# Kernel optimization log

Measured on AMD Instinct MI355X. Metric: run time of the kernel, lower is better.

Reference implementation:

```python
import jax, jax.numpy as jnp
import numpy as np

N = 20000      # nodes
E = 320000     # edges (before self loops)
IN = 128       # in_channels
HID = 64       # hid_channels
H = 4          # in_head
OUT = 16       # out_channels (classes)
SLOPE = 0.2    # GATv2 leaky_relu negative_slope default


def setup_inputs() -> dict:
    key = jax.random.key(0)
    ks = jax.random.split(key, 40)
    d = {}
    d["x"] = jax.random.normal(ks[0], (N, IN), jnp.float32)
    src = jax.random.randint(ks[1], (E,), 0, N)
    dst = jax.random.randint(ks[2], (E,), 0, N)
    d["edge_index"] = jnp.stack([src, dst]).astype(jnp.int32)
    # (in_ch, out_ch_per_head, heads) for the 4 GATv2Conv layers
    dims = [(IN, HID, H), (H * HID, HID, H), (H * HID, HID, H), (H * HID, OUT, 1)]
    ki = 3
    for li, (ic, oc, h) in enumerate(dims, 1):
        sc = 1.0 / np.sqrt(ic)
        d[f"w{li}l"] = jax.random.normal(ks[ki], (h * oc, ic), jnp.float32) * sc; ki += 1
        d[f"b{li}l"] = jnp.zeros((h * oc,), jnp.float32)
        d[f"w{li}r"] = jax.random.normal(ks[ki], (h * oc, ic), jnp.float32) * sc; ki += 1
        d[f"b{li}r"] = jnp.zeros((h * oc,), jnp.float32)
        d[f"a{li}"] = jax.random.normal(ks[ki], (h, oc), jnp.float32) * (1.0 / np.sqrt(oc)); ki += 1
        # output bias: [h*oc] if concat else [oc]; layer 4 is concat=False
        d[f"bo{li}"] = jnp.zeros((h * oc if li < 4 else oc,), jnp.float32)
    return d


def gatv2_layer(x, src, dst, wl, bl, wr, br, att, bias, heads, oc, concat):
    n = x.shape[0]
    xl = (x @ wl.T + bl).reshape(n, heads, oc)   # source transform
    xr = (x @ wr.T + br).reshape(n, heads, oc)   # target transform
    # per-edge GATv2 attention logit: a^T LeakyReLU(x_l[src] + x_r[dst])
    e = jax.nn.leaky_relu(xl[src] + xr[dst], SLOPE)          # [E,H,C]
    logits = jnp.einsum('ehc,hc->eh', e, att)                # [E,H]
    # segment softmax over incoming edges of each dst node
    m = jax.ops.segment_max(logits, dst, num_segments=n)     # [N,H]
    ex = jnp.exp(logits - m[dst])
    den = jax.ops.segment_sum(ex, dst, num_segments=n)
    alpha = ex / den[dst]                                    # [E,H]
    out = jax.ops.segment_sum(alpha[..., None] * xl[src], dst, num_segments=n)  # [N,H,C]
    out = out.reshape(n, heads * oc) if concat else out.mean(axis=1)
    return out + bias


def reference(x, edge_index,
              w1l, b1l, w1r, b1r, a1, bo1,
              w2l, b2l, w2r, b2r, a2, bo2,
              w3l, b3l, w3r, b3r, a3, bo3,
              w4l, b4l, w4r, b4r, a4, bo4):
    n = x.shape[0]
    loop = jnp.arange(n, dtype=edge_index.dtype)
    src = jnp.concatenate([edge_index[0], loop])  # PyG GATv2Conv adds self loops
    dst = jnp.concatenate([edge_index[1], loop])
    h = gatv2_layer(x, src, dst, w1l, b1l, w1r, b1r, a1, bo1, H, HID, True)
    h = jax.nn.relu(h)
    h = gatv2_layer(h, src, dst, w2l, b2l, w2r, b2r, a2, bo2, H, HID, True)
    h = jax.nn.relu(h)
    h = gatv2_layer(h, src, dst, w3l, b3l, w3r, b3r, a3, bo3, H, HID, True)
    h = jax.nn.relu(h)
    h = gatv2_layer(h, src, dst, w4l, b4l, w4r, b4r, a4, bo4, 1, OUT, False)
    return h
```

## Files before the change

kernel.cpp:

```cpp
#include <hip/hip_runtime.h>
#include <hip/hip_bf16.h>
#include <math.h>

#define NNODES 20000
#define NEDGES 320000
#define ETOT   (NEDGES + NNODES)
#define SLOPE  0.2f
#define MAXDEG 96

typedef __attribute__((ext_vector_type(8))) short bf16x8;
typedef __attribute__((ext_vector_type(4))) float f32x4;

__device__ inline unsigned short bfbits(float f) {
    __hip_bfloat16 h = __float2bfloat16(f);
    unsigned short u;
    __builtin_memcpy(&u, &h, 2);
    return u;
}
__device__ inline float bf2f(unsigned short u) {
    __hip_bfloat16 h;
    __builtin_memcpy(&h, &u, 2);
    return __bfloat162float(h);
}

__device__ inline void gload_lds16(const unsigned short* g, unsigned short* s) {
    __builtin_amdgcn_global_load_lds(
        (const __attribute__((address_space(1))) unsigned int*)g,
        (__attribute__((address_space(3))) unsigned int*)s, 16, 0, 0);
}

__global__ void slab_fill(const int* __restrict__ ei, int* __restrict__ fill,
                          int* __restrict__ slab) {
    int idx = blockIdx.x * blockDim.x + threadIdx.x;
    if (idx >= ETOT) return;
    int src, dst;
    if (idx < NEDGES) { src = ei[idx]; dst = ei[NEDGES + idx]; }
    else              { src = idx - NEDGES; dst = src; }
    int pos = atomicAdd(&fill[dst], 1);
    if (pos < MAXDEG) slab[dst * MAXDEG + pos] = src;
}

__global__ void bin_hist(const int* __restrict__ fill, int* __restrict__ bcnt) {
    __shared__ int h[32];
    const int t = threadIdx.x;
    if (t < 32) h[t] = 0;
    __syncthreads();
    int n = blockIdx.x * 256 + t;
    if (n < NNODES) atomicAdd(&h[min(fill[n], 31)], 1);
    __syncthreads();
    if (t < 32 && h[t] > 0) atomicAdd(&bcnt[t], h[t]);
}

__global__ void bin_scan(const int* __restrict__ bcnt, int* __restrict__ bfill) {
    if (threadIdx.x == 0) {
        int run = 0;
        for (int i = 0; i < 32; i++) { bfill[i] = run; run += bcnt[i]; }
    }
}

__global__ void bin_place(const int* __restrict__ fill, int* __restrict__ bfill,
                          int* __restrict__ order) {
    __shared__ int h[32];
    __shared__ int base[32];
    const int t = threadIdx.x;
    if (t < 32) h[t] = 0;
    __syncthreads();
    int n = blockIdx.x * 256 + t;
    int bin = 0, loc = 0;
    if (n < NNODES) {
        bin = min(fill[n], 31);
        loc = atomicAdd(&h[bin], 1);
    }
    __syncthreads();
    if (t < 32) base[t] = (h[t] > 0) ? atomicAdd(&bfill[t], h[t]) : 0;
    __syncthreads();
    if (n < NNODES) order[base[bin] + loc] = n;
}

__global__ void convert_x(const float* __restrict__ x, unsigned short* __restrict__ Ap) {
    int idx = blockIdx.x * 256 + threadIdx.x;
    if (idx >= NNODES * 128) return;
    int m = idx >> 7, k = idx & 127;
    float f = x[idx];
    unsigned short hi = bfbits(f);
    unsigned short lo = bfbits(f - bf2f(hi));
    unsigned short* row = Ap + (size_t)m * 256;
    row[k] = hi; row[128 + k] = lo;
}

__global__ void convert_w(const float* __restrict__ w0, const float* __restrict__ w1,
                          unsigned short* __restrict__ Wp, int K, int n0, int ntot) {
    int idx = blockIdx.x * 256 + threadIdx.x;
    if (idx >= ntot * K) return;
    int n = idx / K, k = idx - n * K;
    float f = (n < n0) ? w0[n * K + k] : w1[(n - n0) * K + k];
    unsigned short hi = bfbits(f);
    unsigned short lo = bfbits(f - bf2f(hi));
    unsigned short* row = Wp + (size_t)n * 2 * K;
    row[k] = hi; row[K + k] = lo;
}

template <int NOUT>
__global__ __launch_bounds__(256) void gemm_mfma(
    const unsigned short* __restrict__ Ap, int KK,
    const unsigned short* __restrict__ Wp,
    const float* __restrict__ bias0, const float* __restrict__ bias1,
    float* __restrict__ O0, float* __restrict__ O1)
{
    __shared__ unsigned short AH[2 * 4096];
    __shared__ unsigned short AL[2 * 4096];
    __shared__ unsigned short BH[2 * 4096];
    __shared__ unsigned short BL[2 * 4096];

    int m0, nblk;
    if constexpr (NOUT == 512) {
        const int bid = blockIdx.x;
        const int xcd = bid & 7;
        const int k   = bid >> 3;
        nblk = k & 3;
        const int g = (k >> 2) * 8 + xcd;
        if (g >= (NNODES + 127) / 128) return;
        m0 = g * 128;
    } else {
        nblk = 0;
        m0 = blockIdx.x * 128;
    }
    const int n0 = nblk * 128;

    const int tid = threadIdx.x;
    const int l   = tid & 63;
    const int wid = tid >> 6;
    const int wr  = wid >> 1;
    const int wc  = wid & 1;

    const int srow = l & 15;
    const int skb  = l >> 4;
    const int W2K  = 2 * KK;

    int arow0 = m0 + wid * 16 + srow;
    int arow1 = arow0 + 64;
    arow0 = min(arow0, NNODES - 1);
    arow1 = min(arow1, NNODES - 1);
    const unsigned short* ahg0 = Ap + (size_t)arow0 * W2K + skb * 8;
    const unsigned short* ahg1 = Ap + (size_t)arow1 * W2K + skb * 8;
    int nrow0 = min(n0 + wid * 16 + srow, NOUT - 1);
    int nrow1 = min(n0 + wid * 16 + srow + 64, NOUT - 1);
    const unsigned short* bhg0 = Wp + (size_t)nrow0 * W2K + skb * 8;
    const unsigned short* bhg1 = Wp + (size_t)nrow1 * W2K + skb * 8;

    const int f0 = (0 * 4 + wid) * 512;
    const int f1 = (1 * 4 + wid) * 512;

    f32x4 acc[4][4];
    #pragma unroll
    for (int i = 0; i < 4; i++)
        #pragma unroll
        for (int j = 0; j < 4; j++)
            acc[i][j] = (f32x4){0.f, 0.f, 0.f, 0.f};

    const int S = KK >> 5;

    auto STAGE = [&](int buf, int k0) {
        const int bo = buf * 4096;
        gload_lds16(ahg0 + k0,      &AH[bo + f0]);
        gload_lds16(ahg1 + k0,      &AH[bo + f1]);
        gload_lds16(ahg0 + KK + k0, &AL[bo + f0]);
        gload_lds16(ahg1 + KK + k0, &AL[bo + f1]);
        gload_lds16(bhg0 + k0,      &BH[bo + f0]);
        gload_lds16(bhg1 + k0,      &BH[bo + f1]);
        gload_lds16(bhg0 + KK + k0, &BL[bo + f0]);
        gload_lds16(bhg1 + KK + k0, &BL[bo + f1]);
    };

    const int ra = (wr * 4) * 512 + l * 8;
    const int rb = (wc * 4) * 512 + l * 8;

    STAGE(0, 0);
    __syncthreads();

    int cur = 0;
    for (int s = 0; s < S; ++s) {
        if (s + 1 < S) STAGE(cur ^ 1, (s + 1) * 32);

        const int bo = cur * 4096;
        bf16x8 ah[4], al_[4], bh[4], bl[4];
        #pragma unroll
        for (int i = 0; i < 4; i++) {
            ah[i]  = *(const bf16x8*)&AH[bo + ra + i * 512];
            al_[i] = *(const bf16x8*)&AL[bo + ra + i * 512];
            bh[i]  = *(const bf16x8*)&BH[bo + rb + i * 512];
            bl[i]  = *(const bf16x8*)&BL[bo + rb + i * 512];
        }

        #pragma unroll
        for (int mi = 0; mi < 4; mi++)
            #pragma unroll
            for (int ni = 0; ni < 4; ni++) {
                acc[mi][ni] = __builtin_amdgcn_mfma_f32_16x16x32_bf16(ah[mi],  bh[ni], acc[mi][ni], 0, 0, 0);
                acc[mi][ni] = __builtin_amdgcn_mfma_f32_16x16x32_bf16(ah[mi],  bl[ni], acc[mi][ni], 0, 0, 0);
                acc[mi][ni] = __builtin_amdgcn_mfma_f32_16x16x32_bf16(al_[mi], bh[ni], acc[mi][ni], 0, 0, 0);
            }

        __syncthreads();
        cur ^= 1;
    }

    if constexpr (NOUT == 512) {
        const bool  left = (nblk < 2);
        float*       O   = left ? O0 : O1;
        const float* bs  = left ? bias0 : bias1;
        const int   cb   = (nblk & 1) * 128;
        #pragma unroll
        for (int mi = 0; mi < 4; mi++) {
            int r0 = m0 + wr * 64 + mi * 16 + (l >> 4) * 4;
            #pragma unroll
            for (int ni = 0; ni < 4; ni++) {
                int c = cb + wc * 64 + ni * 16 + (l & 15);
                int head = c >> 6, ch = c & 63;
                float bv = bs[c];
                #pragma unroll
                for (int r = 0; r < 4; r++) {
                    int m = r0 + r;
                    if (m < NNODES)
                        O[((size_t)head * NNODES + m) * 64 + ch] = acc[mi][ni][r] + bv;
                }
            }
        }
    } else {
        #pragma unroll
        for (int mi = 0; mi < 4; mi++) {
            int r0 = m0 + wr * 64 + mi * 16 + (l >> 4) * 4;
            #pragma unroll
            for (int ni = 0; ni < 4; ni++) {
                int c = wc * 64 + ni * 16 + (l & 15);
                if (c >= 32) continue;
                float bv = (c < 16) ? bias0[c] : bias1[c - 16];
                #pragma unroll
                for (int r = 0; r < 4; r++) {
                    int m = r0 + r;
                    if (m < NNODES) O0[(size_t)m * 32 + c] = acc[mi][ni][r] + bv;
                }
            }
        }
    }
}

__device__ inline float edge_score(float4 v, float4 xrv, float4 attv) {
    float tx = v.x + xrv.x; tx = fmaxf(tx, SLOPE * tx);
    float ty = v.y + xrv.y; ty = fmaxf(ty, SLOPE * ty);
    float tz = v.z + xrv.z; tz = fmaxf(tz, SLOPE * tz);
    float tw = v.w + xrv.w; tw = fmaxf(tw, SLOPE * tw);
    float s = attv.x * tx + attv.y * ty + attv.z * tz + attv.w * tw;
    s += __shfl_xor(s, 1, 64);
    s += __shfl_xor(s, 2, 64);
    s += __shfl_xor(s, 4, 64);
    s += __shfl_xor(s, 8, 64);
    return s;
}

__device__ inline void sm_upd(float s, float4 v, bool act,
                              float& m, float& den, float4& acc) {
    float d = s - m;
    bool  r = act && (d > 8.f);
    float e = __expf(r ? -d : d);
    float sc = r ? e : 1.f;
    float pw = act ? (r ? 1.f : e) : 0.f;
    m = r ? s : m;
    den = den * sc + pw;
    acc.x = acc.x * sc + pw * v.x;
    acc.y = acc.y * sc + pw * v.y;
    acc.z = acc.z * sc + pw * v.z;
    acc.w = acc.w * sc + pw * v.w;
}

__device__ inline void sm_merge(float& m0, float& den0, float4& acc0,
                                float m1, float den1, float4 acc1) {
    float nm = fmaxf(m0, m1);
    float sa = __expf(m0 - nm);
    float sb = __expf(m1 - nm);
    den0 = den0 * sa + den1 * sb;
    acc0.x = acc0.x * sa + acc1.x * sb;
    acc0.y = acc0.y * sa + acc1.y * sb;
    acc0.z = acc0.z * sa + acc1.z * sb;
    acc0.w = acc0.w * sa + acc1.w * sb;
    m0 = nm;
}

__global__ __launch_bounds__(64) void gat_attn_head(
    const float* __restrict__ xl, const float* __restrict__ xr,
    const float* __restrict__ att, const float* __restrict__ bo,
    const int* __restrict__ fill, const int* __restrict__ slab,
    const int* __restrict__ order,
    unsigned short* __restrict__ outp)
{
    const int b    = blockIdx.x;
    const int xcd  = b & 7;
    const int head = xcd >> 1;
    const int grp  = (b >> 3) * 2 + (xcd & 1);
    const int lane = threadIdx.x;
    const int sub  = lane >> 4;
    const int c    = lane & 15;

    const int node = order[grp * 4 + sub];
    const unsigned coff = (unsigned)c << 4;

    const char* xlh = (const char*)xl + (size_t)head * (NNODES * 256);
    const char* xrh = (const char*)xr + (size_t)head * (NNODES * 256);

    const float4 attv = *(const float4*)&att[head * 64 + c * 4];
    const float4 xrv  = *(const float4*)(xrh + ((unsigned)node << 8) + coff);
    const float4 bov  = *(const float4*)&bo[head * 64 + c * 4];

    const int  deg = min(fill[node], MAXDEG);
    const int* sl  = slab + node * MAXDEG;

    int maxd = deg;
    maxd = max(maxd, __shfl_xor(maxd, 16, 64));
    maxd = max(maxd, __shfl_xor(maxd, 32, 64));

    float  m0 = -1e30f, m1 = -1e30f, m2 = -1e30f, m3 = -1e30f;
    float  d0 = 0.f, d1 = 0.f, d2 = 0.f, d3 = 0.f;
    float4 a0 = make_float4(0.f, 0.f, 0.f, 0.f);
    float4 a1 = a0, a2 = a0, a3 = a0;

    auto gather = [&](int src) -> float4 {
        return *(const float4*)(xlh + (((unsigned)src << 8) + coff));
    };

    auto batch = [&](float4 v0, float4 v1, float4 v2, float4 v3, int pb) {
        const bool A0 = pb + 0 < deg, A1 = pb + 1 < deg;
        const bool A2 = pb + 2 < deg, A3 = pb + 3 < deg;
        float s0 = edge_score(v0, xrv, attv);
        float s1 = edge_score(v1, xrv, attv);
        float s2 = edge_score(v2, xrv, attv);
        float s3 = edge_score(v3, xrv, attv);
        bool need = (A0 & (s0 - m0 > 8.f)) | (A1 & (s1 - m1 > 8.f)) |
                    (A2 & (s2 - m2 > 8.f)) | (A3 & (s3 - m3 > 8.f));
        if (!__any(need)) {
            float p0 = A0 ? __expf(s0 - m0) : 0.f;
            float p1 = A1 ? __expf(s1 - m1) : 0.f;
            float p2 = A2 ? __expf(s2 - m2) : 0.f;
            float p3 = A3 ? __expf(s3 - m3) : 0.f;
            d0 += p0; d1 += p1; d2 += p2; d3 += p3;
            a0.x += p0 * v0.x; a0.y += p0 * v0.y; a0.z += p0 * v0.z; a0.w += p0 * v0.w;
            a1.x += p1 * v1.x; a1.y += p1 * v1.y; a1.z += p1 * v1.z; a1.w += p1 * v1.w;
            a2.x += p2 * v2.x; a2.y += p2 * v2.y; a2.z += p2 * v2.z; a2.w += p2 * v2.w;
            a3.x += p3 * v3.x; a3.y += p3 * v3.y; a3.z += p3 * v3.z; a3.w += p3 * v3.w;
        } else {
            sm_upd(s0, v0, A0, m0, d0, a0);
            sm_upd(s1, v1, A1, m1, d1, a1);
            sm_upd(s2, v2, A2, m2, d2, a2);
            sm_upd(s3, v3, A3, m3, d3, a3);
        }
    };

    int4 s4 = *(const int4*)sl;
    float4 v0 = gather((0 < deg) ? s4.x : node);
    float4 v1 = gather((1 < deg) ? s4.y : node);
    float4 v2 = gather((2 < deg) ? s4.z : node);
    float4 v3 = gather((3 < deg) ? s4.w : node);
    int pc = 0;
    for (int p = 4; p < maxd; p += 4) {
        int4 t4 = *(const int4*)&sl[p];
        float4 w0 = gather((p + 0 < deg) ? t4.x : node);
        float4 w1 = gather((p + 1 < deg) ? t4.y : node);
        float4 w2 = gather((p + 2 < deg) ? t4.z : node);
        float4 w3 = gather((p + 3 < deg) ? t4.w : node);
        batch(v0, v1, v2, v3, pc);
        v0 = w0; v1 = w1; v2 = w2; v3 = w3;
        pc = p;
    }
    batch(v0, v1, v2, v3, pc);

    sm_merge(m0, d0, a0, m1, d1, a1);
    sm_merge(m2, d2, a2, m3, d3, a3);
    sm_merge(m0, d0, a0, m2, d2, a2);

    float4 o;
    o.x = fmaxf(a0.x / d0 + bov.x, 0.f);
    o.y = fmaxf(a0.y / d0 + bov.y, 0.f);
    o.z = fmaxf(a0.z / d0 + bov.z, 0.f);
    o.w = fmaxf(a0.w / d0 + bov.w, 0.f);

    unsigned short* row = outp + (size_t)node * 512 + head * 64 + c * 4;
    ushort4 hv, lv;
    hv.x = bfbits(o.x); hv.y = bfbits(o.y); hv.z = bfbits(o.z); hv.w = bfbits(o.w);
    lv.x = bfbits(o.x - bf2f(hv.x));
    lv.y = bfbits(o.y - bf2f(hv.y));
    lv.z = bfbits(o.z - bf2f(hv.z));
    lv.w = bfbits(o.w - bf2f(hv.w));
    *(ushort4*)(row)       = hv;
    *(ushort4*)(row + 256) = lv;
}

__global__ __launch_bounds__(128) void gat_attn_final(
    const float* __restrict__ O32,
    const float* __restrict__ att, const float* __restrict__ bo,
    const int* __restrict__ fill, const int* __restrict__ slab,
    float* __restrict__ out)
{
    const int lane = threadIdx.x & 63;
    const int sub  = lane >> 4;
    const int c    = lane & 15;

    const int node = (blockIdx.x * 2 + (threadIdx.x >> 6)) * 4 + sub;
    if (node >= NNODES) return;

    const unsigned coff = (unsigned)c << 2;
    const char*    ob   = (const char*)O32;

    const float attc = att[c];
    const float xrc  = *(const float*)(ob + (((unsigned)node << 7) + 64 + coff));

    const int  deg = min(fill[node], MAXDEG);
    const int* sl  = slab + node * MAXDEG;

    float m0 = -1e30f, m1 = -1e30f, d0 = 0.f, d1 = 0.f, a0 = 0.f, a1 = 0.f;

    int p = 0;
    for (; p + 2 <= deg; p += 2) {
        int srcA = sl[p];
        int srcB = sl[p + 1];
        float vA = *(const float*)(ob + (((unsigned)srcA << 7) + coff));
        float vB = *(const float*)(ob + (((unsigned)srcB << 7) + coff));
        float tA = vA + xrc; tA = fmaxf(tA, SLOPE * tA);
        float tB = vB + xrc; tB = fmaxf(tB, SLOPE * tB);
        float sA = attc * tA;
        float sB = attc * tB;
        sA += __shfl_xor(sA, 1, 64);  sB += __shfl_xor(sB, 1, 64);
        sA += __shfl_xor(sA, 2, 64);  sB += __shfl_xor(sB, 2, 64);
        sA += __shfl_xor(sA, 4, 64);  sB += __shfl_xor(sB, 4, 64);
        sA += __shfl_xor(sA, 8, 64);  sB += __shfl_xor(sB, 8, 64);
        {
            float dd = sA - m0; bool r = dd > 8.f;
            float e = __expf(r ? -dd : dd);
            float sc = r ? e : 1.f, pw = r ? 1.f : e;
            m0 = r ? sA : m0;
            d0 = d0 * sc + pw;
            a0 = a0 * sc + pw * vA;
        }
        {
            float dd = sB - m1; bool r = dd > 8.f;
            float e = __expf(r ? -dd : dd);
            float sc = r ? e : 1.f, pw = r ? 1.f : e;
            m1 = r ? sB : m1;
            d1 = d1 * sc + pw;
            a1 = a1 * sc + pw * vB;
        }
    }
    if (p < deg) {
        int src = sl[p];
        float v = *(const float*)(ob + (((unsigned)src << 7) + coff));
        float t = v + xrc; t = fmaxf(t, SLOPE * t);
        float s = attc * t;
        s += __shfl_xor(s, 1, 64);
        s += __shfl_xor(s, 2, 64);
        s += __shfl_xor(s, 4, 64);
        s += __shfl_xor(s, 8, 64);
        float dd = s - m0; bool r = dd > 8.f;
        float e = __expf(r ? -dd : dd);
        float sc = r ? e : 1.f, pw = r ? 1.f : e;
        m0 = r ? s : m0;
        d0 = d0 * sc + pw;
        a0 = a0 * sc + pw * v;
    }

    float nm = fmaxf(m0, m1);
    float sa = __expf(m0 - nm);
    float sb = __expf(m1 - nm);
    float den = d0 * sa + d1 * sb;
    out[(size_t)node * 16 + c] = (a0 * sa + a1 * sb) / den + bo[c];
}

extern "C" void kernel_launch(void* const* d_in, const int* in_sizes, int n_in,
                              void* d_out, int out_size, void* d_ws, size_t ws_size,
                              hipStream_t stream)
{
    const float* x   = (const float*)d_in[0];
    const int*   ei  = (const int*)d_in[1];
    const float* w1l = (const float*)d_in[2];  const float* b1l = (const float*)d_in[3];
    const float* w1r = (const float*)d_in[4];  const float* b1r = (const float*)d_in[5];
    const float* a1  = (const float*)d_in[6];  const float* bo1 = (const float*)d_in[7];
    const float* w2l = (const float*)d_in[8];  const float* b2l = (const float*)d_in[9];
    const float* w2r = (const float*)d_in[10]; const float* b2r = (const float*)d_in[11];
    const float* a2  = (const float*)d_in[12]; const float* bo2 = (const float*)d_in[13];
    const float* w3l = (const float*)d_in[14]; const float* b3l = (const float*)d_in[15];
    const float* w3r = (const float*)d_in[16]; const float* b3r = (const float*)d_in[17];
    const float* a3  = (const float*)d_in[18]; const float* bo3 = (const float*)d_in[19];
    const float* w4l = (const float*)d_in[20]; const float* b4l = (const float*)d_in[21];
    const float* w4r = (const float*)d_in[22]; const float* b4r = (const float*)d_in[23];
    const float* a4  = (const float*)d_in[24]; const float* bo4 = (const float*)d_in[25];

    char* ws = (char*)d_ws;
    auto carve = [&](size_t bytes) {
        void* p = ws;
        ws += (bytes + 255) & ~(size_t)255;
        return p;
    };
    unsigned short* Ap = (unsigned short*)carve((size_t)NNODES * 512 * sizeof(unsigned short));
    float* xl = (float*)carve((size_t)NNODES * 256 * sizeof(float));
    float* xr = (float*)carve((size_t)NNODES * 256 * sizeof(float));
    float* O32 = xl;
    unsigned short* Wp1 = (unsigned short*)carve((size_t)512 * 256 * sizeof(unsigned short));
    unsigned short* Wp2 = (unsigned short*)carve((size_t)512 * 512 * sizeof(unsigned short));
    unsigned short* Wp3 = (unsigned short*)carve((size_t)512 * 512 * sizeof(unsigned short));
    unsigned short* Wp4 = (unsigned short*)carve((size_t)32 * 512 * sizeof(unsigned short));
    int* fill  = (int*)carve((size_t)NNODES * sizeof(int));
    int* slab  = (int*)carve((size_t)NNODES * MAXDEG * sizeof(int));
    int* bcnt  = (int*)carve(32 * sizeof(int));
    int* bfill = (int*)carve(32 * sizeof(int));
    int* order = (int*)carve((size_t)NNODES * sizeof(int));

    const int eblocks = (ETOT + 255) / 256;
    const int nblocks = (NNODES + 255) / 256;

    convert_x<<<(NNODES * 128 + 255) / 256, 256, 0, stream>>>(x, Ap);
    convert_w<<<(512 * 128 + 255) / 256, 256, 0, stream>>>(w1l, w1r, Wp1, 128, 256, 512);
    convert_w<<<(512 * 256 + 255) / 256, 256, 0, stream>>>(w2l, w2r, Wp2, 256, 256, 512);
    convert_w<<<(512 * 256 + 255) / 256, 256, 0, stream>>>(w3l, w3r, Wp3, 256, 256, 512);
    convert_w<<<(32 * 256 + 255) / 256, 256, 0, stream>>>(w4l, w4r, Wp4, 256, 16, 32);

    hipMemsetAsync(fill, 0, (size_t)NNODES * sizeof(int), stream);
    hipMemsetAsync(bcnt, 0, 32 * sizeof(int), stream);
    slab_fill<<<eblocks, 256, 0, stream>>>(ei, fill, slab);
    bin_hist<<<nblocks, 256, 0, stream>>>(fill, bcnt);
    bin_scan<<<1, 64, 0, stream>>>(bcnt, bfill);
    bin_place<<<nblocks, 256, 0, stream>>>(fill, bfill, order);

    const int g512 = 640;
    const int ah   = 20000;

    gemm_mfma<512><<<g512, 256, 0, stream>>>(Ap, 128, Wp1, b1l, b1r, xl, xr);
    gat_attn_head<<<ah, 64, 0, stream>>>(xl, xr, a1, bo1, fill, slab, order, Ap);

    gemm_mfma<512><<<g512, 256, 0, stream>>>(Ap, 256, Wp2, b2l, b2r, xl, xr);
    gat_attn_head<<<ah, 64, 0, stream>>>(xl, xr, a2, bo2, fill, slab, order, Ap);

    gemm_mfma<512><<<g512, 256, 0, stream>>>(Ap, 256, Wp3, b3l, b3r, xl, xr);
    gat_attn_head<<<ah, 64, 0, stream>>>(xl, xr, a3, bo3, fill, slab, order, Ap);

    gemm_mfma<32><<<(NNODES + 127) / 128, 256, 0, stream>>>(Ap, 256, Wp4, b4l, b4r, O32, O32);
    gat_attn_final<<<(NNODES + 7) / 8, 128, 0, stream>>>(O32, a4, bo4, fill, slab, (float*)d_out);
}
```

Baseline: 303.2 us.

## Replace LDS-staged GEMM with single-wave register-fed MFMA tiles

The 256-thread, 128x128-tile GEMM that staged A/B through LDS via global_load_lds and block barriers is replaced by a 64-thread kernel. Each wave computes a 64x64 tile (64x32 for the last layer) and loads MFMA operand fragments straight from global memory into double-buffered registers. This removes LDS traffic and __syncthreads, and gives more, smaller blocks for better occupancy and load spread. In exchange, reuse across waves drops, so global and L2 traffic for A and W rises, and register pressure grows.

```diff
diff --git a/kernel.cpp b/kernel.cpp
--- a/kernel.cpp
+++ b/kernel.cpp
@@ -21,12 +21,6 @@
     __hip_bfloat16 h;
     __builtin_memcpy(&h, &u, 2);
     return __bfloat162float(h);
-}
-
-__device__ inline void gload_lds16(const unsigned short* g, unsigned short* s) {
-    __builtin_amdgcn_global_load_lds(
-        (const __attribute__((address_space(1))) unsigned int*)g,
-        (__attribute__((address_space(3))) unsigned int*)s, 16, 0, 0);
 }
 
 __global__ void slab_fill(const int* __restrict__ ei, int* __restrict__ fill,
@@ -100,141 +94,115 @@
     row[k] = hi; row[K + k] = lo;
 }
 
-template <int NOUT>
-__global__ __launch_bounds__(256) void gemm_mfma(
-    const unsigned short* __restrict__ Ap, int KK,
+template <int NOUT, int KK>
+__global__ __launch_bounds__(64) void gemm_reg(
+    const unsigned short* __restrict__ Ap,
     const unsigned short* __restrict__ Wp,
     const float* __restrict__ bias0, const float* __restrict__ bias1,
     float* __restrict__ O0, float* __restrict__ O1)
 {
-    __shared__ unsigned short AH[2 * 4096];
-    __shared__ unsigned short AL[2 * 4096];
-    __shared__ unsigned short BH[2 * 4096];
-    __shared__ unsigned short BL[2 * 4096];
-
-    int m0, nblk;
+    constexpr int S  = KK / 32;
+    constexpr int NF = (NOUT == 512) ? 4 : 2;
+
+    int m0, n0;
     if constexpr (NOUT == 512) {
-        const int bid = blockIdx.x;
-        const int xcd = bid & 7;
-        const int k   = bid >> 3;
-        nblk = k & 3;
-        const int g = (k >> 2) * 8 + xcd;
-        if (g >= (NNODES + 127) / 128) return;
-        m0 = g * 128;
+        const int xcd  = blockIdx.x & 7;
+        const int idx  = blockIdx.x >> 3;
+        const int nblk = idx & 7;
+        const int mg   = idx >> 3;
+        const int mp   = mg * 8 + xcd;
+        if (mp >= (NNODES + 63) / 64) return;
+        m0 = mp * 64;
+        n0 = nblk * 64;
     } else {
-        nblk = 0;
-        m0 = blockIdx.x * 128;
-    }
-    const int n0 = nblk * 128;
-
-    const int tid = threadIdx.x;
-    const int l   = tid & 63;
-    const int wid = tid >> 6;
-    const int wr  = wid >> 1;
-    const int wc  = wid & 1;
-
-    const int srow = l & 15;
-    const int skb  = l >> 4;
-    const int W2K  = 2 * KK;
-
-    int arow0 = m0 + wid * 16 + srow;
-    int arow1 = arow0 + 64;
-    arow0 = min(arow0, NNODES - 1);
-    arow1 = min(arow1, NNODES - 1);
-    const unsigned short* ahg0 = Ap + (size_t)arow0 * W2K + skb * 8;
-    const unsigned short* ahg1 = Ap + (size_t)arow1 * W2K + skb * 8;
-    int nrow0 = min(n0 + wid * 16 + srow, NOUT - 1);
-    int nrow1 = min(n0 + wid * 16 + srow + 64, NOUT - 1);
-    const unsigned short* bhg0 = Wp + (size_t)nrow0 * W2K + skb * 8;
-    const unsigned short* bhg1 = Wp + (size_t)nrow1 * W2K + skb * 8;
-
-    const int f0 = (0 * 4 + wid) * 512;
-    const int f1 = (1 * 4 + wid) * 512;
-
-    f32x4 acc[4][4];
+        m0 = blockIdx.x * 64;
+        n0 = 0;
+    }
+
+    const int l   = threadIdx.x;
+    const int lr  = l & 15;
+    const int lkb = (l >> 4) * 16;
+
+    const char* ab = (const char*)Ap;
+    const char* bb = (const char*)Wp;
+
+    unsigned aoff[4], boff[NF];
+    #pragma unroll
+    for (int f = 0; f < 4; f++) {
+        int row = min(m0 + f * 16 + lr, NNODES - 1);
+        aoff[f] = (unsigned)row * (unsigned)(4 * KK) + (unsigned)lkb;
+    }
+    #pragma unroll
+    for (int f = 0; f < NF; f++) {
+        int row = n0 + f * 16 + lr;
+        boff[f] = (unsigned)row * (unsigned)(4 * KK) + (unsigned)lkb;
+    }
+
+    f32x4 acc[4][NF];
     #pragma unroll
     for (int i = 0; i < 4; i++)
         #pragma unroll
-        for (int j = 0; j < 4; j++)
+        for (int j = 0; j < NF; j++)
             acc[i][j] = (f32x4){0.f, 0.f, 0.f, 0.f};
 
-    const int S = KK >> 5;
-
-    auto STAGE = [&](int buf, int k0) {
-        const int bo = buf * 4096;
-        gload_lds16(ahg0 + k0,      &AH[bo + f0]);
-        gload_lds16(ahg1 + k0,      &AH[bo + f1]);
-        gload_lds16(ahg0 + KK + k0, &AL[bo + f0]);
-        gload_lds16(ahg1 + KK + k0, &AL[bo + f1]);
-        gload_lds16(bhg0 + k0,      &BH[bo + f0]);
-        gload_lds16(bhg1 + k0,      &BH[bo + f1]);
-        gload_lds16(bhg0 + KK + k0, &BL[bo + f0]);
-        gload_lds16(bhg1 + KK + k0, &BL[bo + f1]);
+    bf16x8 fa[2][8];
+    bf16x8 fb[2][2 * NF];
+
+    auto LD = [&](int buf, int s) {
+        const unsigned kb = (unsigned)s * 64;
+        #pragma unroll
+        for (int f = 0; f < 4; f++) {
+            fa[buf][f]     = *(const bf16x8*)(ab + aoff[f] + kb);
+            fa[buf][4 + f] = *(const bf16x8*)(ab + aoff[f] + (unsigned)(2 * KK) + kb);
+        }
+        #pragma unroll
+        for (int f = 0; f < NF; f++) {
+            fb[buf][f]      = *(const bf16x8*)(bb + boff[f] + kb);
+            fb[buf][NF + f] = *(const bf16x8*)(bb + boff[f] + (unsigned)(2 * KK) + kb);
+        }
     };
 
-    const int ra = (wr * 4) * 512 + l * 8;
-    const int rb = (wc * 4) * 512 + l * 8;
-
-    STAGE(0, 0);
-    __syncthreads();
-
-    int cur = 0;
-    for (int s = 0; s < S; ++s) {
-        if (s + 1 < S) STAGE(cur ^ 1, (s + 1) * 32);
-
-        const int bo = cur * 4096;
-        bf16x8 ah[4], al_[4], bh[4], bl[4];
-        #pragma unroll
-        for (int i = 0; i < 4; i++) {
-            ah[i]  = *(const bf16x8*)&AH[bo + ra + i * 512];
-            al_[i] = *(const bf16x8*)&AL[bo + ra + i * 512];
-            bh[i]  = *(const bf16x8*)&BH[bo + rb + i * 512];
-            bl[i]  = *(const bf16x8*)&BL[bo + rb + i * 512];
-        }
-
+    auto COMP = [&](int buf) {
         #pragma unroll
         for (int mi = 0; mi < 4; mi++)
             #pragma unroll
-            for (int ni = 0; ni < 4; ni++) {
-                acc[mi][ni] = __builtin_amdgcn_mfma_f32_16x16x32_bf16(ah[mi],  bh[ni], acc[mi][ni], 0, 0, 0);
-                acc[mi][ni] = __builtin_amdgcn_mfma_f32_16x16x32_bf16(ah[mi],  bl[ni], acc[mi][ni], 0, 0, 0);
-                acc[mi][ni] = __builtin_amdgcn_mfma_f32_16x16x32_bf16(al_[mi], bh[ni], acc[mi][ni], 0, 0, 0);
+            for (int ni = 0; ni < NF; ni++) {
+                acc[mi][ni] = __builtin_amdgcn_mfma_f32_16x16x32_bf16(
+                    fa[buf][mi], fb[buf][ni], acc[mi][ni], 0, 0, 0);
+                acc[mi][ni] = __builtin_amdgcn_mfma_f32_16x16x32_bf16(
+                    fa[buf][mi], fb[buf][NF + ni], acc[mi][ni], 0, 0, 0);
+                acc[mi][ni] = __builtin_amdgcn_mfma_f32_16x16x32_bf16(
+                    fa[buf][4 + mi], fb[buf][ni], acc[mi][ni], 0, 0, 0);
             }
-
-        __syncthreads();
-        cur ^= 1;
-    }
-
-    if constexpr (NOUT == 512) {
-        const bool  left = (nblk < 2);
-        float*       O   = left ? O0 : O1;
-        const float* bs  = left ? bias0 : bias1;
-        const int   cb   = (nblk & 1) * 128;
+    };
+
+    LD(0, 0);
+    #pragma unroll
+    for (int s = 0; s < S; ++s) {
+        if (s + 1 < S) LD((s + 1) & 1, s + 1);
+        COMP(s & 1);
+    }
+
+    #pragma unroll
+    for (int mi = 0; mi < 4; mi++) {
+        int r0 = m0 + mi * 16 + (l >> 4) * 4;
         #pragma unroll
-        for (int mi = 0; mi < 4; mi++) {
-            int r0 = m0 + wr * 64 + mi * 16 + (l >> 4) * 4;
-            #pragma unroll
-            for (int ni = 0; ni < 4; ni++) {
-                int c = cb + wc * 64 + ni * 16 + (l & 15);
-                int head = c >> 6, ch = c & 63;
-                float bv = bs[c];
+        for (int ni = 0; ni < NF; ni++) {
+            int c = n0 + ni * 16 + (l & 15);
+            if constexpr (NOUT == 512) {
+                const bool left = (c < 256);
+                float*       O  = left ? O0 : O1;
+                const int    cc = left ? c : c - 256;
+                const float  bv = left ? bias0[cc] : bias1[cc];
+                const int head = cc >> 6, ch = cc & 63;
                 #pragma unroll
                 for (int r = 0; r < 4; r++) {
                     int m = r0 + r;
                     if (m < NNODES)
                         O[((size_t)head * NNODES + m) * 64 + ch] = acc[mi][ni][r] + bv;
                 }
-            }
-        }
-    } else {
-        #pragma unroll
-        for (int mi = 0; mi < 4; mi++) {
-            int r0 = m0 + wr * 64 + mi * 16 + (l >> 4) * 4;
-            #pragma unroll
-            for (int ni = 0; ni < 4; ni++) {
-                int c = wc * 64 + ni * 16 + (l & 15);
-                if (c >= 32) continue;
-                float bv = (c < 16) ? bias0[c] : bias1[c - 16];
+            } else {
+                const float bv = (c < 16) ? bias0[c] : bias1[c - 16];
                 #pragma unroll
                 for (int r = 0; r < 4; r++) {
                     int m = r0 + r;
@@ -527,18 +495,19 @@
     bin_scan<<<1, 64, 0, stream>>>(bcnt, bfill);
     bin_place<<<nblocks, 256, 0, stream>>>(fill, bfill, order);
 
-    const int g512 = 640;
+    const int g512 = 2560;
+    const int g32  = (NNODES + 63) / 64;
     const int ah   = 20000;
 
-    gemm_mfma<512><<<g512, 256, 0, stream>>>(Ap, 128, Wp1, b1l, b1r, xl, xr);
+    gemm_reg<512, 128><<<g512, 64, 0, stream>>>(Ap, Wp1, b1l, b1r, xl, xr);
     gat_attn_head<<<ah, 64, 0, stream>>>(xl, xr, a1, bo1, fill, slab, order, Ap);
 
-    gemm_mfma<512><<<g512, 256, 0, stream>>>(Ap, 256, Wp2, b2l, b2r, xl, xr);
+    gemm_reg<512, 256><<<g512, 64, 0, stream>>>(Ap, Wp2, b2l, b2r, xl, xr);
     gat_attn_head<<<ah, 64, 0, stream>>>(xl, xr, a2, bo2, fill, slab, order, Ap);
 
-    gemm_mfma<512><<<g512, 256, 0, stream>>>(Ap, 256, Wp3, b3l, b3r, xl, xr);
+    gemm_reg<512, 256><<<g512, 64, 0, stream>>>(Ap, Wp3, b3l, b3r, xl, xr);
     gat_attn_head<<<ah, 64, 0, stream>>>(xl, xr, a3, bo3, fill, slab, order, Ap);
 
-    gemm_mfma<32><<<(NNODES + 127) / 128, 256, 0, stream>>>(Ap, 256, Wp4, b4l, b4r, O32, O32);
+    gemm_reg<32, 256><<<g32, 64, 0, stream>>>(Ap, Wp4, b4l, b4r, O32, O32);
     gat_attn_final<<<(NNODES + 7) / 8, 128, 0, stream>>>(O32, a4, bo4, fill, slab, (float*)d_out);
 }
```

After: 307.6 us. Within noise of the previous version (+1.4%).
